# Optimization experiments

Hardware: AMD Instinct MI355X
Metric: run time of the kernel (lower is better)

## Reference

```python
import jax, jax.numpy as jnp
import numpy as np

HIDDEN = 2048
N_HEADS = 16
HEAD_DIM = HIDDEN // N_HEADS
INV_NORM = 1.0 / float(np.sqrt(HEAD_DIM))
BETA = 1.0


def setup_inputs() -> dict:
    key = jax.random.key(0)
    ks = jax.random.split(key, 12)
    B, S, H = 2, 2048, HIDDEN
    scale = 1.0 / float(np.sqrt(H))
    return {
        "hidden_states": jax.random.normal(ks[0], (B, S, H), jnp.float32),
        "residual": jax.random.normal(ks[1], (B, S, H), jnp.float32),
        "alibi": jax.random.normal(ks[2], (B * N_HEADS, 1, S), jnp.float32),
        "Wq": jax.random.normal(ks[3], (H, H), jnp.float32) * scale,
        "bq": jnp.zeros((H,), jnp.float32),
        "Wk": jax.random.normal(ks[4], (H, H), jnp.float32) * scale,
        "bk": jnp.zeros((H,), jnp.float32),
        "Wv": jax.random.normal(ks[5], (H, H), jnp.float32) * scale,
        "bv": jnp.zeros((H,), jnp.float32),
        "Wd": jax.random.normal(ks[6], (H, H), jnp.float32) * scale,
        "bd": jnp.zeros((H,), jnp.float32),
    }


def reference(hidden_states, residual, alibi, Wq, bq, Wk, bk, Wv, bv, Wd, bd):
    B, S, H = hidden_states.shape
    # separate QKV projections (nn.Linear: x @ W^T + b)
    q = hidden_states @ Wq.T + bq
    k = hidden_states @ Wk.T + bk
    v = hidden_states @ Wv.T + bv
    # [B, n_heads, S, head_dim]
    q = q.reshape(B, S, N_HEADS, HEAD_DIM).transpose(0, 2, 1, 3)
    k = k.reshape(B, S, N_HEADS, HEAD_DIM).transpose(0, 2, 1, 3)
    v = v.reshape(B, S, N_HEADS, HEAD_DIM).transpose(0, 2, 1, 3)
    # baddbmm: scores = beta * alibi + inv_norm * q @ k^T, per (batch*head)
    alibi_bh = alibi.reshape(B, N_HEADS, 1, S)  # broadcasts over query dim
    scores = BETA * alibi_bh + INV_NORM * jnp.einsum("bhqd,bhkd->bhqk", q, k)
    probs = jax.nn.softmax(scores.astype(jnp.float32), axis=-1).astype(v.dtype)
    # attention dropout: p=0.0 (identity)
    ctx = jnp.einsum("bhqk,bhkd->bhqd", probs, v)  # [B,H,S,D]
    ctx = ctx.transpose(0, 2, 1, 3).reshape(B, S, H)
    out = ctx @ Wd.T + bd
    # hidden dropout p=0.0 then residual add (dropout_add)
    return out + residual
```

## Files before the change

### kernel.cpp

```cpp
#include <hip/hip_runtime.h>

#define HID   2048
#define NHEAD 16
#define HD    128
#define SEQ   2048
#define BATCH 2
#define MROWS (BATCH*SEQ)
#define NQKV  (3*HID)
#define INV_NORM 0.08838834764831845f
#define LOG2E    1.4426950408889634f
#define SCALE_L2 (INV_NORM*LOG2E)

typedef __attribute__((ext_vector_type(8)))  __bf16 bf16x8;
typedef __attribute__((ext_vector_type(4)))  float  f32x4;
typedef __attribute__((ext_vector_type(16))) float  f32x16;

typedef __attribute__((address_space(1))) void GV;
typedef __attribute__((address_space(3))) void LV;

__device__ __forceinline__ void async16(const void* g, void* l) {
  __builtin_amdgcn_global_load_lds((const GV*)g, (LV*)l, 16, 0, 0);
}

__device__ __forceinline__ unsigned short f2bf(float f) {
  unsigned u = __builtin_bit_cast(unsigned, f);
  u += 0x7FFFu + ((u >> 16) & 1u);
  return (unsigned short)(u >> 16);
}

__device__ __forceinline__ unsigned pkbf(float a, float b) {
#if __has_builtin(__builtin_amdgcn_cvt_pk_bf16_f32)
  typedef __attribute__((ext_vector_type(2))) __bf16 bf16x2;
  bf16x2 r = __builtin_amdgcn_cvt_pk_bf16_f32(a, b);
  return __builtin_bit_cast(unsigned, r);
#else
  return (unsigned)f2bf(a) | ((unsigned)f2bf(b) << 16);
#endif
}

__device__ __forceinline__ void pl32swap(unsigned &a, unsigned &b) {
#if __has_builtin(__builtin_amdgcn_permlane32_swap)
  typedef __attribute__((ext_vector_type(2))) unsigned u32x2;
  u32x2 r = __builtin_amdgcn_permlane32_swap(a, b, false, false);
  a = r[0]; b = r[1];
#else
  asm volatile("v_permlane32_swap_b32 %0, %1" : "+v"(a), "+v"(b));
#endif
}

__device__ __forceinline__ void mfma16(f32x4& c, bf16x8 a, bf16x8 b) {
  c = __builtin_amdgcn_mfma_f32_16x16x32_bf16(a, b, c, 0, 0, 0);
}

__device__ __forceinline__ bf16x8 frag(const unsigned short* buf, int row, int chunk) {
  return *(const bf16x8*)(buf + ((row * 8 + (chunk ^ (row & 7))) << 3));
}

__global__ __launch_bounds__(256) void cvt_all_kernel(
    const float* __restrict__ hidden,
    const float* __restrict__ W0, const float* __restrict__ W1,
    const float* __restrict__ W2, const float* __restrict__ W3,
    unsigned short* __restrict__ Xb) {
  size_t e = ((size_t)blockIdx.x * 256 + threadIdx.x) * 4;
  const float* src;
  if (e < (size_t)MROWS * HID) {
    src = hidden + e;
  } else {
    size_t r = e - (size_t)MROWS * HID;
    int sel = (int)(r >> 22);
    size_t off = r & ((1u << 22) - 1);
    src = ((sel == 0) ? W0 : (sel == 1) ? W1 : (sel == 2) ? W2 : W3) + off;
  }
  float4 v = *(const float4*)src;
  ushort4 o;
  o.x = f2bf(v.x); o.y = f2bf(v.y); o.z = f2bf(v.z); o.w = f2bf(v.w);
  *(ushort4*)(Xb + e) = o;
}

#define BUFU (24576)
#define BUF3 (3 * BUFU)

__global__ __launch_bounds__(512, 2) void gemm_qkv384_kernel(
    const unsigned short* __restrict__ Xb, const unsigned short* __restrict__ Wb,
    const float* __restrict__ bq, const float* __restrict__ bk,
    const float* __restrict__ bv, unsigned short* __restrict__ Cout,
    unsigned short* __restrict__ Vt) {
  __shared__ __align__(16) unsigned short smem[BUF3];

  const int tid  = threadIdx.x;
  const int w    = tid >> 6;
  const int lane = tid & 63;
  const int l16  = lane & 15;
  const int quad = lane >> 4;
  const int wm   = (w & 3) * 64;
  const int wn   = (w >> 2) * 64;

  const int wg = blockIdx.x;
  const int sw = (wg & 7) * 32 + (wg >> 3);
  const int m0  = (sw & 15) * 256;
  const int rn0 = (sw >> 4) * 384;

  const int sr  = tid >> 3;
  const int scs = ((tid & 7) ^ (sr & 7)) * 8;
  const unsigned short* aBase = Xb + (size_t)(m0 + sr) * HID + scs;

#define STGA(UB, RB, KT)                                              \
  async16(aBase + (size_t)(RB) * HID + (KT),                          \
          (char*)smem + (UB) * 2 + (RB) * 128 + w * 1024)
#define STGB(UB, RB, KT)                                              \
  async16(bBase + (size_t)(RB) * HID + (KT),                          \
          (char*)smem + (UB) * 2 + 32768 + (RB) * 128 + w * 1024)

#define STG6(UB, KT)                                                  \
  { STGA(UB, 0, KT); STGA(UB, 64, KT); STGA(UB, 128, KT);             \
    STGA(UB, 192, KT); STGB(UB, 0, KT); STGB(UB, 64, KT); }

#define VM6  asm volatile("s_waitcnt vmcnt(6)" ::: "memory")
#define VM0  asm volatile("s_waitcnt vmcnt(0)" ::: "memory")

#define PHASE2(UB, STGBLK, WAITBLK)                                            \
  {                                                                            \
    const unsigned short* Ab = smem + (UB);                                    \
    const unsigned short* Bb = Ab + 16384;                                     \
    bf16x8 ta0[4], tb0[4], ta1[4], tb1[4];                                     \
    _Pragma("unroll")                                                          \
    for (int ii = 0; ii < 4; ++ii) ta0[ii] = frag(Ab, wm + ii * 16 + l16, quad); \
    _Pragma("unroll")                                                          \
    for (int j = 0; j < 4; ++j)  tb0[j] = frag(Bb, wn + j * 16 + l16, quad);   \
    _Pragma("unroll")                                                          \
    for (int ii = 0; ii < 4; ++ii) ta1[ii] = frag(Ab, wm + ii * 16 + l16, 4 + quad); \
    _Pragma("unroll")                                                          \
    for (int j = 0; j < 4; ++j)  tb1[j] = frag(Bb, wn + j * 16 + l16, 4 + quad); \
    STGBLK;                                                                    \
    __builtin_amdgcn_s_setprio(1);                                             \
    _Pragma("unroll")                                                          \
    for (int ii = 0; ii < 4; ++ii)                                             \
      _Pragma("unroll")                                                        \
      for (int j = 0; j < 4; ++j) mfma16(acc[ii][j], ta0[ii], tb0[j]);         \
    _Pragma("unroll")                                                          \
    for (int ii = 0; ii < 4; ++ii)                                             \
      _Pragma("unroll")                                                        \
      for (int j = 0; j < 4; ++j) mfma16(acc[ii][j], ta1[ii], tb1[j]);         \
    __builtin_amdgcn_s_setprio(0);                                             \
    asm volatile("s_waitcnt lgkmcnt(0)" ::: "memory");                         \
    WAITBLK;                                                                   \
    __builtin_amdgcn_s_barrier();                                              \
  }

  for (int p = 0; p < 3; ++p) {
    const unsigned short* bBase = Wb + (size_t)(rn0 + p * 128 + sr) * HID + scs;

    f32x4 acc[4][4];
    const f32x4 zero = {0.f, 0.f, 0.f, 0.f};
#pragma unroll
    for (int a = 0; a < 4; ++a)
#pragma unroll
      for (int j = 0; j < 4; ++j) acc[a][j] = zero;

    STG6(0, 0);
    STG6(BUFU, 64);
    VM6;
    __builtin_amdgcn_s_barrier();

    int kb = 0;
    for (int g = 0; g < 10; ++g) {
      PHASE2(0,        STG6(2*BUFU, kb+128), VM6);
      PHASE2(BUFU,     STG6(0,      kb+192), VM6);
      PHASE2(2*BUFU,   STG6(BUFU,   kb+256), VM6);
      kb += 192;
    }
    PHASE2(0,    {}, VM0);
    PHASE2(BUFU, {}, {});

#pragma unroll
    for (int j = 0; j < 4; ++j) {
      int ng = rn0 + p * 128 + wn + j * 16 + l16;
      float bias = (ng < HID) ? bq[ng] : (ng < 2 * HID ? bk[ng - HID] : bv[ng - 2 * HID]);
      if (Vt != nullptr && ng >= 2 * HID) {
        const int vidx = ng - 2 * HID;
        const int bb = m0 >> 11;
        unsigned short* vrow = Vt
            + ((size_t)((bb * 16 + (vidx >> 7)) * 128 + (vidx & 127))) * SEQ
            + (m0 & 2047) + wm + quad * 4;
#pragma unroll
        for (int a = 0; a < 4; ++a) {
          ushort4 pk4;
          pk4.x = f2bf(acc[a][j][0] + bias);
          pk4.y = f2bf(acc[a][j][1] + bias);
          pk4.z = f2bf(acc[a][j][2] + bias);
          pk4.w = f2bf(acc[a][j][3] + bias);
          *(ushort4*)(vrow + a * 16) = pk4;
        }
      } else {
#pragma unroll
        for (int a = 0; a < 4; ++a)
#pragma unroll
          for (int r = 0; r < 4; ++r) {
            int mg = m0 + wm + a * 16 + quad * 4 + r;
            Cout[(size_t)mg * NQKV + ng] = f2bf(acc[a][j][r] + bias);
          }
      }
    }
  }
#undef STGA
#undef STGB
#undef STG6
#undef PHASE2
#undef VM6
#undef VM0
}

__global__ __launch_bounds__(512, 2) void gemm_out384_kernel(
    const unsigned short* __restrict__ Ctx, const unsigned short* __restrict__ Wdb,
    const float* __restrict__ bd, const float* __restrict__ Res,
    float* __restrict__ Out) {
  __shared__ __align__(16) unsigned short smem[BUF3];

  const int tid  = threadIdx.x;
  const int w    = tid >> 6;
  const int lane = tid & 63;
  const int l16  = lane & 15;
  const int quad = lane >> 4;
  const int wm   = (w & 3) * 64;
  const int wn   = (w >> 2) * 64;

  const int wg = blockIdx.x;
  const int sw = (wg & 7) * 32 + (wg >> 3);
  const int m0  = (sw & 15) * 256;
  const int rn0 = (sw >> 4) * 128;

  const int sr  = tid >> 3;
  const int scs = ((tid & 7) ^ (sr & 7)) * 8;
  const unsigned short* aBase = Ctx + (size_t)(m0 + sr) * HID + scs;
  const unsigned short* bBase = Wdb + (size_t)(rn0 + sr) * HID + scs;

#define STGA(UB, RB, KT)                                              \
  async16(aBase + (size_t)(RB) * HID + (KT),                          \
          (char*)smem + (UB) * 2 + (RB) * 128 + w * 1024)
#define STGB(UB, RB, KT)                                              \
  async16(bBase + (size_t)(RB) * HID + (KT),                          \
          (char*)smem + (UB) * 2 + 32768 + (RB) * 128 + w * 1024)

#define STG6(UB, KT)                                                  \
  { STGA(UB, 0, KT); STGA(UB, 64, KT); STGA(UB, 128, KT);             \
    STGA(UB, 192, KT); STGB(UB, 0, KT); STGB(UB, 64, KT); }

#define VM6  asm volatile("s_waitcnt vmcnt(6)" ::: "memory")
#define VM0  asm volatile("s_waitcnt vmcnt(0)" ::: "memory")

#define PHASE2(UB, STGBLK, WAITBLK)                                            \
  {                                                                            \
    const unsigned short* Ab = smem + (UB);                                    \
    const unsigned short* Bb = Ab + 16384;                                     \
    bf16x8 ta0[4], tb0[4], ta1[4], tb1[4];                                     \
    _Pragma("unroll")                                                          \
    for (int ii = 0; ii < 4; ++ii) ta0[ii] = frag(Ab, wm + ii * 16 + l16, quad); \
    _Pragma("unroll")                                                          \
    for (int j = 0; j < 4; ++j)  tb0[j] = frag(Bb, wn + j * 16 + l16, quad);   \
    _Pragma("unroll")                                                          \
    for (int ii = 0; ii < 4; ++ii) ta1[ii] = frag(Ab, wm + ii * 16 + l16, 4 + quad); \
    _Pragma("unroll")                                                          \
    for (int j = 0; j < 4; ++j)  tb1[j] = frag(Bb, wn + j * 16 + l16, 4 + quad); \
    STGBLK;                                                                    \
    __builtin_amdgcn_s_setprio(1);                                             \
    _Pragma("unroll")                                                          \
    for (int ii = 0; ii < 4; ++ii)                                             \
      _Pragma("unroll")                                                        \
      for (int j = 0; j < 4; ++j) mfma16(acc[ii][j], ta0[ii], tb0[j]);         \
    _Pragma("unroll")                                                          \
    for (int ii = 0; ii < 4; ++ii)                                             \
      _Pragma("unroll")                                                        \
      for (int j = 0; j < 4; ++j) mfma16(acc[ii][j], ta1[ii], tb1[j]);         \
    __builtin_amdgcn_s_setprio(0);                                             \
    asm volatile("s_waitcnt lgkmcnt(0)" ::: "memory");                         \
    WAITBLK;                                                                   \
    __builtin_amdgcn_s_barrier();                                              \
  }

  f32x4 acc[4][4];
  const f32x4 zero = {0.f, 0.f, 0.f, 0.f};
#pragma unroll
  for (int a = 0; a < 4; ++a)
#pragma unroll
    for (int j = 0; j < 4; ++j) acc[a][j] = zero;

  STG6(0, 0);
  STG6(BUFU, 64);
  VM6;
  __builtin_amdgcn_s_barrier();

  int kb = 0;
  for (int g = 0; g < 10; ++g) {
    PHASE2(0,        STG6(2*BUFU, kb+128), VM6);
    PHASE2(BUFU,     STG6(0,      kb+192), VM6);
    PHASE2(2*BUFU,   STG6(BUFU,   kb+256), VM6);
    kb += 192;
  }
  PHASE2(0,    {}, VM0);
  PHASE2(BUFU, {}, {});

#pragma unroll
  for (int j = 0; j < 4; ++j) {
    int ng = rn0 + wn + j * 16 + l16;
    float bias = bd[ng];
#pragma unroll
    for (int a = 0; a < 4; ++a)
#pragma unroll
      for (int r = 0; r < 4; ++r) {
        int mg = m0 + wm + a * 16 + quad * 4 + r;
        size_t off = (size_t)mg * HID + ng;
        Out[off] = acc[a][j][r] + bias + Res[off];
      }
  }
#undef STGA
#undef STGB
#undef STG6
#undef PHASE2
#undef VM6
#undef VM0
}

__global__ __launch_bounds__(256) void vtrans_kernel(const unsigned short* __restrict__ QKV,
                                                     unsigned short* __restrict__ Vt) {
  __shared__ __align__(16) unsigned short T[64][72];
  const int s0 = blockIdx.x * 64, d0 = blockIdx.y * 64, bh = blockIdx.z;
  const int b = bh >> 4, h = bh & 15;
  const int tid = threadIdx.x;
#pragma unroll
  for (int i = 0; i < 2; ++i) {
    int idx = i * 256 + tid;
    int r = idx >> 3, ch = idx & 7;
    const unsigned short* g = QKV + ((size_t)b * SEQ + s0 + r) * NQKV + 2 * HID + h * HD + d0 + ch * 8;
    *(uint4*)(&T[r][ch * 8]) = *(const uint4*)g;
  }
  __syncthreads();
#pragma unroll
  for (int i = 0; i < 2; ++i) {
    int idx = i * 256 + tid;
    int d = idx >> 3, ch = idx & 7;
    unsigned short v[8];
#pragma unroll
    for (int x = 0; x < 8; ++x) v[x] = T[ch * 8 + x][d];
    unsigned short* g = Vt + ((size_t)bh * HD + d0 + d) * SEQ + s0 + ch * 8;
    *(uint4*)g = *(const uint4*)v;
  }
}

__global__ __launch_bounds__(512, 2) void attn_kernel(
    const unsigned short* __restrict__ QKV, const unsigned short* __restrict__ Vt,
    const float* __restrict__ alibi, unsigned short* __restrict__ Ctx) {
  __shared__ __align__(16) char smem[73728];
  unsigned short* Ks0  = (unsigned short*)smem;
  unsigned short* Ks1  = (unsigned short*)(smem + 16384);
  unsigned short* Vts0 = (unsigned short*)(smem + 32768);
  unsigned short* Vts1 = (unsigned short*)(smem + 49152);
  float*          Alsf = (float*)(smem + 65536);
  unsigned short* Qs   = (unsigned short*)smem;

  const int tid = threadIdx.x, w = tid >> 6, lane = tid & 63;
  const int l32 = lane & 31, h = lane >> 5;
  const int bid = blockIdx.x;
  const int t  = bid >> 3;
  const int q0 = (t & 7) * 256;
  const int bh = (bid & 7) + 8 * (t >> 3);
  const int b = bh >> 4, hh = bh & 15;
  const size_t rowbase = (size_t)b * SEQ;
  const float* ali = alibi + (size_t)bh * SEQ;
  const unsigned short* Vbh = Vt + (size_t)bh * HD * SEQ;

  {
    const unsigned short* qbase = QKV + (rowbase + q0) * NQKV + hh * HD;
#pragma unroll
    for (int i = 0; i < 8; ++i) {
      int slot = i * 512 + w * 64 + lane;
      int r = slot >> 4, c = (slot & 15) ^ (r & 15);
      async16(qbase + (size_t)r * NQKV + c * 8, (char*)Qs + (size_t)(i * 512 + w * 64) * 16);
    }
    async16((const char*)ali + (size_t)(w * 64 + lane) * 16, (char*)Alsf + (size_t)(w * 64) * 16);
  }
  __syncthreads();
  bf16x8 qf[8];
  {
    int qr = w * 32 + l32;
#pragma unroll
    for (int ks = 0; ks < 8; ++ks) {
      int c = (ks * 2 + h) ^ (qr & 15);
      qf[ks] = *(const bf16x8*)(Qs + (qr * 16 + c) * 8);
    }
  }

  f32x16 oacc[4];
  float l_acc = 0.f;
#pragma unroll
  for (int nb = 0; nb < 4; ++nb)
#pragma unroll
    for (int r = 0; r < 16; ++r) oacc[nb][r] = 0.f;

  __syncthreads();

#define STAGE_K(T, KD)                                                           \
  {                                                                              \
    const unsigned short* kbase = QKV + (rowbase + (size_t)(T) * 64) * NQKV + HID + hh * HD; \
    _Pragma("unroll")                                                            \
    for (int i = 0; i < 2; ++i) {                                                \
      int slot = i * 512 + w * 64 + lane;                                        \
      int r = slot >> 4, c = (slot & 15) ^ (r & 15);                             \
      async16(kbase + (size_t)r * NQKV + c * 8, (char*)(KD) + (size_t)(i * 512 + w * 64) * 16); \
    }                                                                            \
  }
#define STAGE_V(T, VD)                                                           \
  {                                                                              \
    const unsigned short* vbase = Vbh + (T) * 64;                                \
    _Pragma("unroll")                                                            \
    for (int i = 0; i < 2; ++i) {                                                \
      int slot = i * 512 + w * 64 + lane;                                        \
      int r = slot >> 3, c = (slot & 7) ^ (r & 7);                               \
      async16(vbase + (size_t)r * SEQ + c * 8, (char*)(VD) + (size_t)(i * 512 + w * 64) * 16); \
    }                                                                            \
  }

#define QKT(SACC, KBUF)                                                          \
  {                                                                              \
    _Pragma("unroll")                                                            \
    for (int mb = 0; mb < 2; ++mb)                                               \
      _Pragma("unroll")                                                          \
      for (int r = 0; r < 16; ++r) (SACC)[mb][r] = 0.f;                          \
    __builtin_amdgcn_s_setprio(1);                                               \
    _Pragma("unroll")                                                            \
    for (int ks = 0; ks < 8; ++ks)                                               \
      _Pragma("unroll")                                                          \
      for (int mb = 0; mb < 2; ++mb) {                                           \
        bf16x8 kf = *(const bf16x8*)((KBUF) + ((mb * 32 + l32) * 16 + ((ks * 2 + h) ^ (l32 & 15))) * 8); \
        (SACC)[mb] = __builtin_amdgcn_mfma_f32_32x32x16_bf16(kf, qf[ks], (SACC)[mb], 0, 0, 0); \
      }                                                                          \
    __builtin_amdgcn_s_setprio(0);                                               \
  }

#define SOFTMAX(SACC, KT, PFR)                                                   \
  {                                                                              \
    const float* alsk = Alsf + (KT) * 64 + 4 * h;                                \
    _Pragma("unroll")                                                            \
    for (int mb = 0; mb < 2; ++mb) {                                             \
      float p[16];                                                               \
      _Pragma("unroll")                                                          \
      for (int g = 0; g < 4; ++g) {                                              \
        float4 av = *(const float4*)(alsk + mb * 32 + g * 8);                    \
        p[g * 4 + 0] = __builtin_amdgcn_exp2f((SACC)[mb][g * 4 + 0] * SCALE_L2 + av.x * LOG2E); \
        p[g * 4 + 1] = __builtin_amdgcn_exp2f((SACC)[mb][g * 4 + 1] * SCALE_L2 + av.y * LOG2E); \
        p[g * 4 + 2] = __builtin_amdgcn_exp2f((SACC)[mb][g * 4 + 2] * SCALE_L2 + av.z * LOG2E); \
        p[g * 4 + 3] = __builtin_amdgcn_exp2f((SACC)[mb][g * 4 + 3] * SCALE_L2 + av.w * LOG2E); \
        l_acc += (p[g * 4 + 0] + p[g * 4 + 1]) + (p[g * 4 + 2] + p[g * 4 + 3]);  \
      }                                                                          \
      unsigned c0 = pkbf(p[0],  p[1]),  c1 = pkbf(p[2],  p[3]);                  \
      unsigned c2 = pkbf(p[4],  p[5]),  c3 = pkbf(p[6],  p[7]);                  \
      unsigned c4 = pkbf(p[8],  p[9]),  c5 = pkbf(p[10], p[11]);                 \
      unsigned c6 = pkbf(p[12], p[13]), c7 = pkbf(p[14], p[15]);                 \
      pl32swap(c0, c2);  pl32swap(c1, c3);                                       \
      pl32swap(c4, c6);  pl32swap(c5, c7);                                       \
      uint4 f0; f0.x = c0; f0.y = c1; f0.z = c2; f0.w = c3;                      \
      uint4 f1; f1.x = c4; f1.y = c5; f1.z = c6; f1.w = c7;                      \
      (PFR)[mb * 2 + 0] = __builtin_bit_cast(bf16x8, f0);                        \
      (PFR)[mb * 2 + 1] = __builtin_bit_cast(bf16x8, f1);                        \
    }                                                                            \
  }

#define PVOP(PFR, VBUF)                                                          \
  {                                                                              \
    __builtin_amdgcn_s_setprio(1);                                               \
    _Pragma("unroll")                                                            \
    for (int ks2 = 0; ks2 < 4; ++ks2) {                                          \
      bf16x8 pf = (PFR)[ks2];                                                    \
      _Pragma("unroll")                                                          \
      for (int nb = 0; nb < 4; ++nb) {                                           \
        bf16x8 vf = *(const bf16x8*)((VBUF) + ((nb * 32 + l32) * 8 + ((ks2 * 2 + h) ^ (l32 & 7))) * 8); \
        oacc[nb] = __builtin_amdgcn_mfma_f32_32x32x16_bf16(pf, vf, oacc[nb], 0, 0, 0); \
      }                                                                          \
    }                                                                            \
    __builtin_amdgcn_s_setprio(0);                                               \
  }

  STAGE_K(0, Ks0);  STAGE_V(0, Vts0);
  STAGE_K(1, Ks1);  STAGE_V(1, Vts1);
  asm volatile("s_waitcnt vmcnt(4)" ::: "memory");
  __builtin_amdgcn_s_barrier();

  f32x16 sA[2], sB[2];
  QKT(sA, Ks0);
  asm volatile("s_waitcnt lgkmcnt(0)" ::: "memory");
  __builtin_amdgcn_s_barrier();

  for (int kt = 0; kt < 30; kt += 2) {
    STAGE_K(kt + 2, Ks0);
    asm volatile("s_waitcnt vmcnt(4)" ::: "memory");
    QKT(sB, Ks1);
    { bf16x8 pfr[4]; SOFTMAX(sA, kt, pfr); PVOP(pfr, Vts0); }
    asm volatile("s_waitcnt lgkmcnt(0)" ::: "memory");
    __builtin_amdgcn_s_barrier();
    STAGE_V(kt + 2, Vts0);
    STAGE_K(kt + 3, Ks1);
    asm volatile("s_waitcnt vmcnt(4)" ::: "memory");
    QKT(sA, Ks0);
    { bf16x8 pfr[4]; SOFTMAX(sB, kt + 1, pfr); PVOP(pfr, Vts1); }
    asm volatile("s_waitcnt lgkmcnt(0)" ::: "memory");
    __builtin_amdgcn_s_barrier();
    STAGE_V(kt + 3, Vts1);
  }

  asm volatile("s_waitcnt vmcnt(2)" ::: "memory");
  QKT(sB, Ks1);
  { bf16x8 pfr[4]; SOFTMAX(sA, 30, pfr); PVOP(pfr, Vts0); }
  asm volatile("s_waitcnt lgkmcnt(0) vmcnt(0)" ::: "memory");
  __builtin_amdgcn_s_barrier();
  { bf16x8 pfr[4]; SOFTMAX(sB, 31, pfr); PVOP(pfr, Vts1); }
  asm volatile("s_waitcnt lgkmcnt(0)" ::: "memory");

#undef STAGE_K
#undef STAGE_V
#undef QKT
#undef SOFTMAX
#undef PVOP

  float lf = l_acc + __shfl_xor(l_acc, 32, 64);
  float rinv[16];
#pragma unroll
  for (int reg = 0; reg < 16; ++reg) {
    int row = (reg & 3) + 8 * (reg >> 2) + 4 * h;
    rinv[reg] = 1.0f / __shfl(lf, row, 64);
  }

#pragma unroll
  for (int nb = 0; nb < 4; ++nb)
#pragma unroll
    for (int reg = 0; reg < 16; ++reg) {
      int row = (reg & 3) + 8 * (reg >> 2) + 4 * h;
      size_t qg = rowbase + q0 + w * 32 + row;
      Ctx[qg * HID + hh * HD + nb * 32 + l32] = f2bf(oacc[nb][reg] * rinv[reg]);
    }
}

extern "C" void kernel_launch(void* const* d_in, const int* in_sizes, int n_in,
                              void* d_out, int out_size, void* d_ws, size_t ws_size,
                              hipStream_t stream) {
  const float* hidden   = (const float*)d_in[0];
  const float* residual = (const float*)d_in[1];
  const float* alibi    = (const float*)d_in[2];
  const float* Wq = (const float*)d_in[3];
  const float* bq = (const float*)d_in[4];
  const float* Wk = (const float*)d_in[5];
  const float* bk = (const float*)d_in[6];
  const float* Wv = (const float*)d_in[7];
  const float* bv = (const float*)d_in[8];
  const float* Wd = (const float*)d_in[9];
  const float* bd = (const float*)d_in[10];
  float* out = (float*)d_out;

  unsigned short* Xb    = (unsigned short*)d_ws;
  unsigned short* Wqkvb = Xb + (size_t)MROWS * HID;
  unsigned short* Wdb   = Wqkvb + (size_t)NQKV * HID;
  unsigned short* QKVb  = Wdb + (size_t)HID * HID;
  unsigned short* Ctxb  = QKVb + (size_t)MROWS * NQKV;
  unsigned short* VtF   = Ctxb + (size_t)MROWS * HID;

  const size_t needU = (size_t)MROWS * HID + (size_t)NQKV * HID + (size_t)HID * HID
                     + (size_t)MROWS * NQKV + (size_t)MROWS * HID
                     + (size_t)BATCH * NHEAD * HD * SEQ;
  const bool fused = ws_size >= needU * sizeof(unsigned short);

  const int nTot = (MROWS * HID + 4 * HID * HID) / 4 / 256;
  cvt_all_kernel<<<nTot, 256, 0, stream>>>(hidden, Wq, Wk, Wv, Wd, Xb);

  if (fused) {
    gemm_qkv384_kernel<<<256, 512, 0, stream>>>(Xb, Wqkvb, bq, bk, bv, QKVb, VtF);
    attn_kernel<<<256, 512, 0, stream>>>(QKVb, VtF, alibi, Ctxb);
  } else {
    unsigned short* Vtb = Wqkvb;
    gemm_qkv384_kernel<<<256, 512, 0, stream>>>(Xb, Wqkvb, bq, bk, bv, QKVb, nullptr);
    vtrans_kernel<<<dim3(SEQ / 64, HD / 64, BATCH * NHEAD), 256, 0, stream>>>(QKVb, Vtb);
    attn_kernel<<<256, 512, 0, stream>>>(QKVb, Vtb, alibi, Ctxb);
  }
  gemm_out384_kernel<<<256, 512, 0, stream>>>(Ctxb, Wdb, bd, residual, out);
}
```

Measured before the change: 396.2 us.

## Shrink GEMM tiles to 128x128 with 256-thread blocks and double buffering

Both projection GEMMs move from 256-row tiles with 512 threads and a triple-buffered LDS pipeline to 128-row tiles with 256 threads and a two-stage buffer, launching twice as many workgroups. The aim is more workgroups per CU and better load balance across the 256 CUs, with less LDS per block. In exchange, each loaded B tile is reused less, and waiting on vmcnt(0) every tile removes most of the load/compute overlap the deeper pipeline provided.

Result: slower. 421.2 us (+6.3%).

```diff
diff --git a/kernel.cpp b/kernel.cpp
--- a/kernel.cpp
+++ b/kernel.cpp
@@ -77,51 +77,24 @@
   *(ushort4*)(Xb + e) = o;
 }
 
-#define BUFU (24576)
-#define BUF3 (3 * BUFU)
-
-__global__ __launch_bounds__(512, 2) void gemm_qkv384_kernel(
-    const unsigned short* __restrict__ Xb, const unsigned short* __restrict__ Wb,
-    const float* __restrict__ bq, const float* __restrict__ bk,
-    const float* __restrict__ bv, unsigned short* __restrict__ Cout,
-    unsigned short* __restrict__ Vt) {
-  __shared__ __align__(16) unsigned short smem[BUF3];
-
-  const int tid  = threadIdx.x;
-  const int w    = tid >> 6;
-  const int lane = tid & 63;
-  const int l16  = lane & 15;
-  const int quad = lane >> 4;
-  const int wm   = (w & 3) * 64;
-  const int wn   = (w >> 2) * 64;
-
-  const int wg = blockIdx.x;
-  const int sw = (wg & 7) * 32 + (wg >> 3);
-  const int m0  = (sw & 15) * 256;
-  const int rn0 = (sw >> 4) * 384;
-
-  const int sr  = tid >> 3;
-  const int scs = ((tid & 7) ^ (sr & 7)) * 8;
-  const unsigned short* aBase = Xb + (size_t)(m0 + sr) * HID + scs;
-
-#define STGA(UB, RB, KT)                                              \
+#define QBUF 16384
+
+#define GSTGA(UB, RB, KT)                                             \
   async16(aBase + (size_t)(RB) * HID + (KT),                          \
-          (char*)smem + (UB) * 2 + (RB) * 128 + w * 1024)
-#define STGB(UB, RB, KT)                                              \
+          (char*)smem + (UB) * 2 + (RB) * 128 + tid * 16)
+#define GSTGB(UB, RB, KT)                                             \
   async16(bBase + (size_t)(RB) * HID + (KT),                          \
-          (char*)smem + (UB) * 2 + 32768 + (RB) * 128 + w * 1024)
-
-#define STG6(UB, KT)                                                  \
-  { STGA(UB, 0, KT); STGA(UB, 64, KT); STGA(UB, 128, KT);             \
-    STGA(UB, 192, KT); STGB(UB, 0, KT); STGB(UB, 64, KT); }
-
-#define VM6  asm volatile("s_waitcnt vmcnt(6)" ::: "memory")
-#define VM0  asm volatile("s_waitcnt vmcnt(0)" ::: "memory")
-
-#define PHASE2(UB, STGBLK, WAITBLK)                                            \
+          (char*)smem + (UB) * 2 + 16384 + (RB) * 128 + tid * 16)
+#define GSTG8(UB, KT)                                                 \
+  { GSTGA(UB, 0, KT); GSTGA(UB, 32, KT); GSTGA(UB, 64, KT); GSTGA(UB, 96, KT); \
+    GSTGB(UB, 0, KT); GSTGB(UB, 32, KT); GSTGB(UB, 64, KT); GSTGB(UB, 96, KT); }
+
+#define GVM0  asm volatile("s_waitcnt vmcnt(0)" ::: "memory")
+
+#define GTILE(UB, STGBLK, WAITBLK)                                             \
   {                                                                            \
     const unsigned short* Ab = smem + (UB);                                    \
-    const unsigned short* Bb = Ab + 16384;                                     \
+    const unsigned short* Bb = Ab + 8192;                                      \
     bf16x8 ta0[4], tb0[4], ta1[4], tb1[4];                                     \
     _Pragma("unroll")                                                          \
     for (int ii = 0; ii < 4; ++ii) ta0[ii] = frag(Ab, wm + ii * 16 + l16, quad); \
@@ -147,6 +120,30 @@
     __builtin_amdgcn_s_barrier();                                              \
   }
 
+__global__ __launch_bounds__(256, 2) void gemm_qkv128_kernel(
+    const unsigned short* __restrict__ Xb, const unsigned short* __restrict__ Wb,
+    const float* __restrict__ bq, const float* __restrict__ bk,
+    const float* __restrict__ bv, unsigned short* __restrict__ Cout,
+    unsigned short* __restrict__ Vt) {
+  __shared__ __align__(16) unsigned short smem[2 * QBUF];
+
+  const int tid  = threadIdx.x;
+  const int w    = tid >> 6;
+  const int lane = tid & 63;
+  const int l16  = lane & 15;
+  const int quad = lane >> 4;
+  const int wm   = (w & 1) * 64;
+  const int wn   = (w >> 1) * 64;
+
+  const int wg = blockIdx.x;
+  const int sw = (wg & 7) * 64 + (wg >> 3);
+  const int m0  = (sw & 31) * 128;
+  const int rn0 = (sw >> 5) * 384;
+
+  const int sr  = tid >> 3;
+  const int scs = ((tid & 7) ^ (sr & 7)) * 8;
+  const unsigned short* aBase = Xb + (size_t)(m0 + sr) * HID + scs;
+
   for (int p = 0; p < 3; ++p) {
     const unsigned short* bBase = Wb + (size_t)(rn0 + p * 128 + sr) * HID + scs;
 
@@ -157,20 +154,18 @@
 #pragma unroll
       for (int j = 0; j < 4; ++j) acc[a][j] = zero;
 
-    STG6(0, 0);
-    STG6(BUFU, 64);
-    VM6;
+    GSTG8(0, 0);
+    GVM0;
     __builtin_amdgcn_s_barrier();
 
     int kb = 0;
-    for (int g = 0; g < 10; ++g) {
-      PHASE2(0,        STG6(2*BUFU, kb+128), VM6);
-      PHASE2(BUFU,     STG6(0,      kb+192), VM6);
-      PHASE2(2*BUFU,   STG6(BUFU,   kb+256), VM6);
-      kb += 192;
+    for (int g = 0; g < 15; ++g) {
+      GTILE(0,    GSTG8(QBUF, kb + 64),  GVM0);
+      GTILE(QBUF, GSTG8(0,    kb + 128), GVM0);
+      kb += 128;
     }
-    PHASE2(0,    {}, VM0);
-    PHASE2(BUFU, {}, {});
+    GTILE(0,    GSTG8(QBUF, kb + 64), GVM0);
+    GTILE(QBUF, {}, {});
 
 #pragma unroll
     for (int j = 0; j < 4; ++j) {
@@ -201,82 +196,34 @@
           }
       }
     }
-  }
-#undef STGA
-#undef STGB
-#undef STG6
-#undef PHASE2
-#undef VM6
-#undef VM0
-}
-
-__global__ __launch_bounds__(512, 2) void gemm_out384_kernel(
+    __builtin_amdgcn_s_barrier();
+  }
+}
+
+__global__ __launch_bounds__(256, 2) void gemm_out128_kernel(
     const unsigned short* __restrict__ Ctx, const unsigned short* __restrict__ Wdb,
     const float* __restrict__ bd, const float* __restrict__ Res,
     float* __restrict__ Out) {
-  __shared__ __align__(16) unsigned short smem[BUF3];
+  __shared__ __align__(16) unsigned short smem[2 * QBUF];
 
   const int tid  = threadIdx.x;
   const int w    = tid >> 6;
   const int lane = tid & 63;
   const int l16  = lane & 15;
   const int quad = lane >> 4;
-  const int wm   = (w & 3) * 64;
-  const int wn   = (w >> 2) * 64;
+  const int wm   = (w & 1) * 64;
+  const int wn   = (w >> 1) * 64;
 
   const int wg = blockIdx.x;
-  const int sw = (wg & 7) * 32 + (wg >> 3);
-  const int m0  = (sw & 15) * 256;
-  const int rn0 = (sw >> 4) * 128;
+  const int sw = (wg & 7) * 64 + (wg >> 3);
+  const int m0  = (sw & 31) * 128;
+  const int rn0 = (sw >> 5) * 128;
 
   const int sr  = tid >> 3;
   const int scs = ((tid & 7) ^ (sr & 7)) * 8;
   const unsigned short* aBase = Ctx + (size_t)(m0 + sr) * HID + scs;
   const unsigned short* bBase = Wdb + (size_t)(rn0 + sr) * HID + scs;
 
-#define STGA(UB, RB, KT)                                              \
-  async16(aBase + (size_t)(RB) * HID + (KT),                          \
-          (char*)smem + (UB) * 2 + (RB) * 128 + w * 1024)
-#define STGB(UB, RB, KT)                                              \
-  async16(bBase + (size_t)(RB) * HID + (KT),                          \
-          (char*)smem + (UB) * 2 + 32768 + (RB) * 128 + w * 1024)
-
-#define STG6(UB, KT)                                                  \
-  { STGA(UB, 0, KT); STGA(UB, 64, KT); STGA(UB, 128, KT);             \
-    STGA(UB, 192, KT); STGB(UB, 0, KT); STGB(UB, 64, KT); }
-
-#define VM6  asm volatile("s_waitcnt vmcnt(6)" ::: "memory")
-#define VM0  asm volatile("s_waitcnt vmcnt(0)" ::: "memory")
-
-#define PHASE2(UB, STGBLK, WAITBLK)                                            \
-  {                                                                            \
-    const unsigned short* Ab = smem + (UB);                                    \
-    const unsigned short* Bb = Ab + 16384;                                     \
-    bf16x8 ta0[4], tb0[4], ta1[4], tb1[4];                                     \
-    _Pragma("unroll")                                                          \
-    for (int ii = 0; ii < 4; ++ii) ta0[ii] = frag(Ab, wm + ii * 16 + l16, quad); \
-    _Pragma("unroll")                                                          \
-    for (int j = 0; j < 4; ++j)  tb0[j] = frag(Bb, wn + j * 16 + l16, quad);   \
-    _Pragma("unroll")                                                          \
-    for (int ii = 0; ii < 4; ++ii) ta1[ii] = frag(Ab, wm + ii * 16 + l16, 4 + quad); \
-    _Pragma("unroll")                                                          \
-    for (int j = 0; j < 4; ++j)  tb1[j] = frag(Bb, wn + j * 16 + l16, 4 + quad); \
-    STGBLK;                                                                    \
-    __builtin_amdgcn_s_setprio(1);                                             \
-    _Pragma("unroll")                                                          \
-    for (int ii = 0; ii < 4; ++ii)                                             \
-      _Pragma("unroll")                                                        \
-      for (int j = 0; j < 4; ++j) mfma16(acc[ii][j], ta0[ii], tb0[j]);         \
-    _Pragma("unroll")                                                          \
-    for (int ii = 0; ii < 4; ++ii)                                             \
-      _Pragma("unroll")                                                        \
-      for (int j = 0; j < 4; ++j) mfma16(acc[ii][j], ta1[ii], tb1[j]);         \
-    __builtin_amdgcn_s_setprio(0);                                             \
-    asm volatile("s_waitcnt lgkmcnt(0)" ::: "memory");                         \
-    WAITBLK;                                                                   \
-    __builtin_amdgcn_s_barrier();                                              \
-  }
-
   f32x4 acc[4][4];
   const f32x4 zero = {0.f, 0.f, 0.f, 0.f};
 #pragma unroll
@@ -284,20 +231,18 @@
 #pragma unroll
     for (int j = 0; j < 4; ++j) acc[a][j] = zero;
 
-  STG6(0, 0);
-  STG6(BUFU, 64);
-  VM6;
+  GSTG8(0, 0);
+  GVM0;
   __builtin_amdgcn_s_barrier();
 
   int kb = 0;
-  for (int g = 0; g < 10; ++g) {
-    PHASE2(0,        STG6(2*BUFU, kb+128), VM6);
-    PHASE2(BUFU,     STG6(0,      kb+192), VM6);
-    PHASE2(2*BUFU,   STG6(BUFU,   kb+256), VM6);
-    kb += 192;
-  }
-  PHASE2(0,    {}, VM0);
-  PHASE2(BUFU, {}, {});
+  for (int g = 0; g < 15; ++g) {
+    GTILE(0,    GSTG8(QBUF, kb + 64),  GVM0);
+    GTILE(QBUF, GSTG8(0,    kb + 128), GVM0);
+    kb += 128;
+  }
+  GTILE(0,    GSTG8(QBUF, kb + 64), GVM0);
+  GTILE(QBUF, {}, {});
 
 #pragma unroll
   for (int j = 0; j < 4; ++j) {
@@ -312,12 +257,6 @@
         Out[off] = acc[a][j][r] + bias + Res[off];
       }
   }
-#undef STGA
-#undef STGB
-#undef STG6
-#undef PHASE2
-#undef VM6
-#undef VM0
 }
 
 __global__ __launch_bounds__(256) void vtrans_kernel(const unsigned short* __restrict__ QKV,
@@ -570,13 +509,13 @@
   cvt_all_kernel<<<nTot, 256, 0, stream>>>(hidden, Wq, Wk, Wv, Wd, Xb);
 
   if (fused) {
-    gemm_qkv384_kernel<<<256, 512, 0, stream>>>(Xb, Wqkvb, bq, bk, bv, QKVb, VtF);
+    gemm_qkv128_kernel<<<512, 256, 0, stream>>>(Xb, Wqkvb, bq, bk, bv, QKVb, VtF);
     attn_kernel<<<256, 512, 0, stream>>>(QKVb, VtF, alibi, Ctxb);
   } else {
     unsigned short* Vtb = Wqkvb;
-    gemm_qkv384_kernel<<<256, 512, 0, stream>>>(Xb, Wqkvb, bq, bk, bv, QKVb, nullptr);
+    gemm_qkv128_kernel<<<512, 256, 0, stream>>>(Xb, Wqkvb, bq, bk, bv, QKVb, nullptr);
     vtrans_kernel<<<dim3(SEQ / 64, HD / 64, BATCH * NHEAD), 256, 0, stream>>>(QKVb, Vtb);
     attn_kernel<<<256, 512, 0, stream>>>(QKVb, Vtb, alibi, Ctxb);
   }
-  gemm_out384_kernel<<<256, 512, 0, stream>>>(Ctxb, Wdb, bd, residual, out);
-}
+  gemm_out128_kernel<<<512, 256, 0, stream>>>(Ctxb, Wdb, bd, residual, out);
+}
```
